# Performance work log

Measured on AMD Instinct MI355X. Metric: run time of the kernel, lower is better.

## Reference

```python
import jax, jax.numpy as jnp
import numpy as np

NUM_LAYERS = 24
LN_EPS = 1e-5


def setup_inputs() -> dict:
    key = jax.random.key(0)
    ks = jax.random.split(key, 8)
    B, S = 256, 8192
    x = jax.random.uniform(ks[0], (B, S, 5), dtype=jnp.float32)
    # per-layer LayerNorm(4) params (torch default init: weight=1, bias=0; use
    # randomized values so the gather is non-trivial)
    ln_w = 1.0 + 0.1 * jax.random.normal(ks[1], (NUM_LAYERS, 4), dtype=jnp.float32)
    ln_b = 0.1 * jax.random.normal(ks[2], (NUM_LAYERS, 4), dtype=jnp.float32)
    # MLP 5 -> 64 -> 32 -> 1 (dropout inactive in eval mode)
    W1 = jax.random.normal(ks[3], (64, 5), dtype=jnp.float32) / np.sqrt(5)
    b1 = jnp.zeros((64,), dtype=jnp.float32)
    W2 = jax.random.normal(ks[4], (32, 64), dtype=jnp.float32) / np.sqrt(64)
    b2 = jnp.zeros((32,), dtype=jnp.float32)
    W3 = jax.random.normal(ks[5], (1, 32), dtype=jnp.float32) / np.sqrt(32)
    b3 = jnp.zeros((1,), dtype=jnp.float32)
    return {"x": x, "ln_w": ln_w, "ln_b": ln_b, "W1": W1, "b1": b1,
            "W2": W2, "b2": b2, "W3": W3, "b3": b3}


def reference(x, ln_w, ln_b, W1, b1, W2, b2, W3, b3):
    B, S, _ = x.shape
    x_flat = x.reshape(-1, 5)                      # [N, 5]
    layer_pos = x_flat[:, -1]                      # [N]
    layer_ids = jnp.clip((layer_pos * NUM_LAYERS).astype(jnp.int32), 0, NUM_LAYERS - 1)
    feats = x_flat[:, :4]                          # [N, 4]
    # vectorized per-token LayerNorm: gather per-token gamma/beta by layer id
    mean = jnp.mean(feats, axis=-1, keepdims=True)
    var = jnp.mean(jnp.square(feats - mean), axis=-1, keepdims=True)  # biased, as torch LN
    normed = (feats - mean) * jax.lax.rsqrt(var + LN_EPS)
    normed = normed * ln_w[layer_ids] + ln_b[layer_ids]               # [N, 4]
    x_norm = jnp.concatenate([normed, layer_pos[:, None]], axis=1)    # [N, 5]
    h = jax.nn.relu(x_norm @ W1.T + b1)            # [N, 64]
    h = jax.nn.relu(h @ W2.T + b2)                 # [N, 32]
    scores = h @ W3.T + b3                         # [N, 1]
    return scores.reshape(B, S)
```

## Files before the change

kernel.cpp:

```cpp
#include <hip/hip_runtime.h>
#include <hip/hip_bf16.h>
#include <stdint.h>

#define NUM_LAYERS 24
#define LN_EPS 1e-5f
#define N_ROWS (256 * 8192)
#define ROWS_PER_ITER 64
#define NUM_ITERS (N_ROWS / ROWS_PER_ITER)
#define NUM_BLOCKS 768

typedef __attribute__((ext_vector_type(4)))  uint32_t u32x4;
typedef __attribute__((ext_vector_type(16))) float    f32x16;
typedef __attribute__((ext_vector_type(2)))  float    f32x2;
typedef __attribute__((ext_vector_type(2)))  __fp16   h16x2;

__device__ __forceinline__ uint32_t pk_f16_rtz(float lo, float hi) {
    h16x2 v = __builtin_amdgcn_cvt_pkrtz(lo, hi);
    uint32_t u; __builtin_memcpy(&u, &v, 4);
    return u;
}
__device__ __forceinline__ uint32_t pk_f16_rne(float lo, float hi) {
    __fp16 a = (__fp16)lo, b = (__fp16)hi;
    uint16_t ua, ub;
    __builtin_memcpy(&ua, &a, 2); __builtin_memcpy(&ub, &b, 2);
    return (uint32_t)ua | ((uint32_t)ub << 16);
}
__device__ __forceinline__ uint32_t pk_relu_f16(uint32_t d) {
    h16x2 v; __builtin_memcpy(&v, &d, 4);
    h16x2 z = {(__fp16)0.0f, (__fp16)0.0f};
    v = __builtin_elementwise_max(v, z);
    uint32_t u; __builtin_memcpy(&u, &v, 4);
    return u;
}

__device__ __forceinline__ u32x4 make_frag(uint32_t d0, uint32_t d1,
                                           uint32_t d2, uint32_t d3) {
    u32x4 f; f.x = d0; f.y = d1; f.z = d2; f.w = d3;
    return f;
}

__device__ __forceinline__ f32x16 mfma_f16_c(u32x4 a, u32x4 b, const f32x16& c) {
    f32x16 d;
    asm("s_nop 2\n\tv_mfma_f32_32x32x16_f16 %0, %1, %2, %3"
        : "=&v"(d) : "v"(a), "v"(b), "v"(c));
    return d;
}
__device__ __forceinline__ f32x16 mfma_f16_z(u32x4 a, u32x4 b) {
    f32x16 d;
    asm("s_nop 2\n\tv_mfma_f32_32x32x16_f16 %0, %1, %2, 0"
        : "=&v"(d) : "v"(a), "v"(b));
    return d;
}
__device__ __forceinline__ void mfma_f16_acc(f32x16& c, u32x4 a, u32x4 b) {
    asm("s_nop 2\n\tv_mfma_f32_32x32x16_f16 %0, %1, %2, %0"
        : "+v"(c) : "v"(a), "v"(b));
}
__device__ __forceinline__ void mfma_fence2(f32x16& c0, f32x16& c1) {
    asm volatile("s_nop 7\n\ts_nop 7\n\ts_nop 7" : "+v"(c0), "+v"(c1));
}
__device__ __forceinline__ void mfma_fence4(f32x16& c0, f32x16& c1,
                                            f32x16& c2, f32x16& c3) {
    asm volatile("s_nop 7\n\ts_nop 7\n\ts_nop 7"
                 : "+v"(c0), "+v"(c1), "+v"(c2), "+v"(c3));
}

__device__ __forceinline__ int sigma_k(int p) {
    int hh = (p >> 2) & 1;
    int base = (p & 31) - 4 * hh;
    int r = (base & 3) + 4 * (base >> 3);
    return 32 * (p >> 5) + 16 * (r >> 3) + 8 * hh + (r & 7);
}

__global__ __launch_bounds__(256, 3) void router_mfma(
    const float* __restrict__ x,
    const float* __restrict__ ln_w,
    const float* __restrict__ ln_b,
    const float* __restrict__ W1,
    const float* __restrict__ b1,
    const float* __restrict__ W2,
    const float* __restrict__ b2,
    const float* __restrict__ W3,
    const float* __restrict__ b3,
    float* __restrict__ out)
{
    __shared__ float s_ln[NUM_LAYERS * 8];
    const int t = threadIdx.x;
    if (t < NUM_LAYERS * 4) {
        int lid = t >> 2, c = t & 3;
        s_ln[lid * 8 + c]     = ln_w[t];
        s_ln[lid * 8 + 4 + c] = ln_b[t];
    }
    __syncthreads();

    const int lane = t & 63;
    const int wid  = t >> 6;
    const int n32  = lane & 31;
    const int h    = lane >> 5;

    u32x4 a1f[2];
#pragma unroll
    for (int mt = 0; mt < 2; ++mt) {
        int p = mt * 32 + n32;
        int k = sigma_k(p);
        uint32_t d0 = pk_f16_rne(W1[k * 5 + 0], W1[k * 5 + 1]);
        uint32_t d1 = pk_f16_rne(W1[k * 5 + 2], W1[k * 5 + 3]);
        uint32_t d2 = pk_f16_rne(W1[k * 5 + 4], b1[k]);
        if (h) { d0 = 0; d1 = 0; d2 = 0; }
        a1f[mt] = make_frag(d0, d1, d2, 0);
    }

    u32x4 w2f[4];
#pragma unroll
    for (int kt = 0; kt < 4; ++kt) {
        const float* wp = W2 + n32 * 64 + kt * 16 + h * 8;
        const float4 lo = *(const float4*)(wp);
        const float4 hi = *(const float4*)(wp + 4);
        w2f[kt] = make_frag(pk_f16_rne(lo.x, lo.y), pk_f16_rne(lo.z, lo.w),
                            pk_f16_rne(hi.x, hi.y), pk_f16_rne(hi.z, hi.w));
    }

    f32x16 c2init;
    f32x2 w3p[8];
#pragma unroll
    for (int r2 = 0; r2 < 8; ++r2) {
        const int n = ((2 * r2) & 3) + 8 * (r2 >> 1) + 4 * h;
        w3p[r2] = f32x2{W3[n], W3[n + 1]};
        c2init[2 * r2]     = b2[n];
        c2init[2 * r2 + 1] = b2[n + 1];
    }
    const float b3v = b3[0];
    const f32x2 z2 = {0.0f, 0.0f};

    const int total_waves = NUM_BLOCKS * 4;
    const int w = blockIdx.x * 4 + wid;

    int it = w;
    const float* xp0 = x + (size_t)(it * ROWS_PER_ITER + lane) * 5;
    float f0 = xp0[0], f1 = xp0[1], f2 = xp0[2], f3 = xp0[3], lp = xp0[4];

    while (true) {
        const int nit = it + total_waves;
        const bool more = nit < NUM_ITERS;
        const float* nxp =
            x + (size_t)((more ? nit : it) * ROWS_PER_ITER + lane) * 5;
        const float nf0 = nxp[0], nf1 = nxp[1], nf2 = nxp[2], nf3 = nxp[3],
                    nlp = nxp[4];

        const int rowBase = it * ROWS_PER_ITER;

        int lid = (int)(lp * (float)NUM_LAYERS);
        lid = lid < 0 ? 0 : (lid > NUM_LAYERS - 1 ? NUM_LAYERS - 1 : lid);

        const float m  = (f0 + f1 + f2 + f3) * 0.25f;
        const float d0 = f0 - m, d1 = f1 - m, d2 = f2 - m, d3 = f3 - m;
        const float var = (d0 * d0 + d1 * d1 + d2 * d2 + d3 * d3) * 0.25f;
        const float r   = rsqrtf(var + LN_EPS);

        const float4 g  = *(const float4*)(s_ln + lid * 8);
        const float4 bb = *(const float4*)(s_ln + lid * 8 + 4);

        const float xn0 = fmaf(d0 * r, g.x, bb.x);
        const float xn1 = fmaf(d1 * r, g.y, bb.y);
        const float xn2 = fmaf(d2 * r, g.z, bb.z);
        const float xn3 = fmaf(d3 * r, g.w, bb.w);

        const uint32_t e0 = pk_f16_rtz(xn0, xn1);
        const uint32_t e1 = pk_f16_rtz(xn2, xn3);
        const uint32_t e2 = pk_f16_rtz(lp, 1.0f);
        const uint32_t x0 = __shfl_xor((int)e0, 32, 64);
        const uint32_t x1 = __shfl_xor((int)e1, 32, 64);
        const uint32_t x2 = __shfl_xor((int)e2, 32, 64);

        const u32x4 bf_t0 = make_frag(e0, e1, e2, 0u);
        const u32x4 bf_t1 = make_frag(x0, x1, x2, 0u);

        f32x16 c1a0 = mfma_f16_z(a1f[0], bf_t0);
        f32x16 c1b0 = mfma_f16_z(a1f[1], bf_t0);
        f32x16 c1a1 = mfma_f16_z(a1f[0], bf_t1);
        f32x16 c1b1 = mfma_f16_z(a1f[1], bf_t1);
        mfma_fence4(c1a0, c1b0, c1a1, c1b1);

        u32x4 h1f0[4], h1f1[4];
#pragma unroll
        for (int kt = 0; kt < 4; ++kt) {
            const f32x16& c1 = (kt < 2) ? c1a0 : c1b0;
            const int roff = 8 * (kt & 1);
            uint32_t dw[4];
#pragma unroll
            for (int d = 0; d < 4; ++d)
                dw[d] = pk_relu_f16(
                    pk_f16_rtz(c1[roff + 2 * d], c1[roff + 2 * d + 1]));
            h1f0[kt] = make_frag(dw[0], dw[1], dw[2], dw[3]);
        }
#pragma unroll
        for (int kt = 0; kt < 4; ++kt) {
            const f32x16& c1 = (kt < 2) ? c1a1 : c1b1;
            const int roff = 8 * (kt & 1);
            uint32_t dw[4];
#pragma unroll
            for (int d = 0; d < 4; ++d)
                dw[d] = pk_relu_f16(
                    pk_f16_rtz(c1[roff + 2 * d], c1[roff + 2 * d + 1]));
            h1f1[kt] = make_frag(dw[0], dw[1], dw[2], dw[3]);
        }

        f32x16 c2_0 = mfma_f16_c(w2f[0], h1f0[0], c2init);
        f32x16 c2_1 = mfma_f16_c(w2f[0], h1f1[0], c2init);
#pragma unroll
        for (int kt = 1; kt < 4; ++kt) {
            mfma_f16_acc(c2_0, w2f[kt], h1f0[kt]);
            mfma_f16_acc(c2_1, w2f[kt], h1f1[kt]);
        }
        mfma_fence2(c2_0, c2_1);

        f32x2 acc0 = z2, acc1 = z2;
#pragma unroll
        for (int r2 = 0; r2 < 8; ++r2) {
            f32x2 v0 = {c2_0[2 * r2], c2_0[2 * r2 + 1]};
            f32x2 v1 = {c2_1[2 * r2], c2_1[2 * r2 + 1]};
            v0 = __builtin_elementwise_max(v0, z2);
            v1 = __builtin_elementwise_max(v1, z2);
            acc0 = v0 * w3p[r2] + acc0;
            acc1 = v1 * w3p[r2] + acc1;
        }
        float p0 = acc0.x + acc0.y;
        float p1 = acc1.x + acc1.y;
        p0 += __shfl_xor(p0, 32, 64);
        p1 += __shfl_xor(p1, 32, 64);

        out[rowBase + lane] = (h ? p1 : p0) + b3v;

        if (!more) break;
        it = nit;
        f0 = nf0; f1 = nf1; f2 = nf2; f3 = nf3; lp = nlp;
    }
}

extern "C" void kernel_launch(void* const* d_in, const int* in_sizes, int n_in,
                              void* d_out, int out_size, void* d_ws, size_t ws_size,
                              hipStream_t stream) {
    const float* x    = (const float*)d_in[0];
    const float* ln_w = (const float*)d_in[1];
    const float* ln_b = (const float*)d_in[2];
    const float* W1   = (const float*)d_in[3];
    const float* b1   = (const float*)d_in[4];
    const float* W2   = (const float*)d_in[5];
    const float* b2   = (const float*)d_in[6];
    const float* W3   = (const float*)d_in[7];
    const float* b3   = (const float*)d_in[8];
    float* out = (float*)d_out;

    router_mfma<<<NUM_BLOCKS, 256, 0, stream>>>(x, ln_w, ln_b, W1, b1, W2, b2,
                                                W3, b3, out);
}
```

Baseline: 108.8 us.

## Coalesce x loads via LDS staging, batch MFMA asm, raise block count

Each wave now loads its 64-row chunk of x with contiguous, coalesced 4-byte loads (stride 64 per pass) and stages it through a per-wave LDS buffer before reading per-row features, instead of strided 5-float per-lane loads. The MFMA calls are merged into two multi-instruction asm blocks so there are fewer s_nop hazard pads, the LayerNorm params are stored transposed in LDS and use the hardware rsq builtin, and the grid grows from 768 to 2048 blocks. This adds LDS traffic, relies on intra-wave ordering of the LDS writes and reads without a barrier, and raises register pressure from the large asm operand lists.

Measured after the change: 108.3 us. No clear change (-0.4%).

```diff
diff --git a/kernel.cpp b/kernel.cpp
--- a/kernel.cpp
+++ b/kernel.cpp
@@ -1,5 +1,4 @@
 #include <hip/hip_runtime.h>
-#include <hip/hip_bf16.h>
 #include <stdint.h>
 
 #define NUM_LAYERS 24
@@ -7,7 +6,7 @@
 #define N_ROWS (256 * 8192)
 #define ROWS_PER_ITER 64
 #define NUM_ITERS (N_ROWS / ROWS_PER_ITER)
-#define NUM_BLOCKS 768
+#define NUM_BLOCKS 2048
 
 typedef __attribute__((ext_vector_type(4)))  uint32_t u32x4;
 typedef __attribute__((ext_vector_type(16))) float    f32x16;
@@ -39,21 +38,38 @@
     return f;
 }
 
-__device__ __forceinline__ f32x16 mfma_f16_c(u32x4 a, u32x4 b, const f32x16& c) {
-    f32x16 d;
-    asm("s_nop 2\n\tv_mfma_f32_32x32x16_f16 %0, %1, %2, %3"
-        : "=&v"(d) : "v"(a), "v"(b), "v"(c));
-    return d;
-}
-__device__ __forceinline__ f32x16 mfma_f16_z(u32x4 a, u32x4 b) {
-    f32x16 d;
-    asm("s_nop 2\n\tv_mfma_f32_32x32x16_f16 %0, %1, %2, 0"
-        : "=&v"(d) : "v"(a), "v"(b));
-    return d;
-}
-__device__ __forceinline__ void mfma_f16_acc(f32x16& c, u32x4 a, u32x4 b) {
-    asm("s_nop 2\n\tv_mfma_f32_32x32x16_f16 %0, %1, %2, %0"
-        : "+v"(c) : "v"(a), "v"(b));
+__device__ __forceinline__ void mfma_l1(f32x16& d0, f32x16& d1,
+                                        f32x16& d2, f32x16& d3,
+                                        const u32x4& a0, const u32x4& a1,
+                                        const u32x4& b0, const u32x4& b1) {
+    asm("s_nop 2\n\t"
+        "v_mfma_f32_32x32x16_f16 %0, %4, %6, 0\n\t"
+        "v_mfma_f32_32x32x16_f16 %1, %5, %6, 0\n\t"
+        "v_mfma_f32_32x32x16_f16 %2, %4, %7, 0\n\t"
+        "v_mfma_f32_32x32x16_f16 %3, %5, %7, 0"
+        : "=&v"(d0), "=&v"(d1), "=&v"(d2), "=&v"(d3)
+        : "v"(a0), "v"(a1), "v"(b0), "v"(b1));
+}
+__device__ __forceinline__ void mfma_l2(f32x16& c0, f32x16& c1, const f32x16& cinit,
+                                        const u32x4& w0, const u32x4& w1,
+                                        const u32x4& w2, const u32x4& w3,
+                                        const u32x4& h00, const u32x4& h01,
+                                        const u32x4& h02, const u32x4& h03,
+                                        const u32x4& h10, const u32x4& h11,
+                                        const u32x4& h12, const u32x4& h13) {
+    asm("s_nop 2\n\t"
+        "v_mfma_f32_32x32x16_f16 %0, %3, %7, %2\n\t"
+        "v_mfma_f32_32x32x16_f16 %1, %3, %11, %2\n\t"
+        "v_mfma_f32_32x32x16_f16 %0, %4, %8, %0\n\t"
+        "v_mfma_f32_32x32x16_f16 %1, %4, %12, %1\n\t"
+        "v_mfma_f32_32x32x16_f16 %0, %5, %9, %0\n\t"
+        "v_mfma_f32_32x32x16_f16 %1, %5, %13, %1\n\t"
+        "v_mfma_f32_32x32x16_f16 %0, %6, %10, %0\n\t"
+        "v_mfma_f32_32x32x16_f16 %1, %6, %14, %1"
+        : "=&v"(c0), "=&v"(c1)
+        : "v"(cinit), "v"(w0), "v"(w1), "v"(w2), "v"(w3),
+          "v"(h00), "v"(h01), "v"(h02), "v"(h03),
+          "v"(h10), "v"(h11), "v"(h12), "v"(h13));
 }
 __device__ __forceinline__ void mfma_fence2(f32x16& c0, f32x16& c1) {
     asm volatile("s_nop 7\n\ts_nop 7\n\ts_nop 7" : "+v"(c0), "+v"(c1));
@@ -83,12 +99,14 @@
     const float* __restrict__ b3,
     float* __restrict__ out)
 {
-    __shared__ float s_ln[NUM_LAYERS * 8];
+    __shared__ float s_ln[8 * NUM_LAYERS];
+    __shared__ float s_x[4][ROWS_PER_ITER * 5];
+
     const int t = threadIdx.x;
-    if (t < NUM_LAYERS * 4) {
-        int lid = t >> 2, c = t & 3;
-        s_ln[lid * 8 + c]     = ln_w[t];
-        s_ln[lid * 8 + 4 + c] = ln_b[t];
+    if (t < 8 * NUM_LAYERS) {
+        const int q = t & 7, lid = t >> 3;
+        s_ln[q * NUM_LAYERS + lid] =
+            (q < 4) ? ln_w[lid * 4 + q] : ln_b[lid * 4 + (q - 4)];
     }
     __syncthreads();
 
@@ -134,17 +152,27 @@
     const int total_waves = NUM_BLOCKS * 4;
     const int w = blockIdx.x * 4 + wid;
 
+    float* const sx = &s_x[wid][0];
+    const float* const sxr = sx + 5 * lane;
+
     int it = w;
-    const float* xp0 = x + (size_t)(it * ROWS_PER_ITER + lane) * 5;
-    float f0 = xp0[0], f1 = xp0[1], f2 = xp0[2], f3 = xp0[3], lp = xp0[4];
+    {
+        const float* xg = x + (size_t)it * (ROWS_PER_ITER * 5);
+        float ld[5];
+#pragma unroll
+        for (int j = 0; j < 5; ++j) ld[j] = xg[j * 64 + lane];
+#pragma unroll
+        for (int j = 0; j < 5; ++j) sx[j * 64 + lane] = ld[j];
+    }
+    float f0 = sxr[0], f1 = sxr[1], f2 = sxr[2], f3 = sxr[3], lp = sxr[4];
 
     while (true) {
         const int nit = it + total_waves;
         const bool more = nit < NUM_ITERS;
-        const float* nxp =
-            x + (size_t)((more ? nit : it) * ROWS_PER_ITER + lane) * 5;
-        const float nf0 = nxp[0], nf1 = nxp[1], nf2 = nxp[2], nf3 = nxp[3],
-                    nlp = nxp[4];
+        const float* xg = x + (size_t)(more ? nit : it) * (ROWS_PER_ITER * 5);
+        float ld[5];
+#pragma unroll
+        for (int j = 0; j < 5; ++j) ld[j] = xg[j * 64 + lane];
 
         const int rowBase = it * ROWS_PER_ITER;
 
@@ -154,15 +182,19 @@
         const float m  = (f0 + f1 + f2 + f3) * 0.25f;
         const float d0 = f0 - m, d1 = f1 - m, d2 = f2 - m, d3 = f3 - m;
         const float var = (d0 * d0 + d1 * d1 + d2 * d2 + d3 * d3) * 0.25f;
-        const float r   = rsqrtf(var + LN_EPS);
-
-        const float4 g  = *(const float4*)(s_ln + lid * 8);
-        const float4 bb = *(const float4*)(s_ln + lid * 8 + 4);
-
-        const float xn0 = fmaf(d0 * r, g.x, bb.x);
-        const float xn1 = fmaf(d1 * r, g.y, bb.y);
-        const float xn2 = fmaf(d2 * r, g.z, bb.z);
-        const float xn3 = fmaf(d3 * r, g.w, bb.w);
+#if __has_builtin(__builtin_amdgcn_rsqf)
+        const float r = __builtin_amdgcn_rsqf(var + LN_EPS);
+#else
+        const float r = rsqrtf(var + LN_EPS);
+#endif
+        const float rg0 = r * s_ln[0 * 24 + lid];
+        const float rg1 = r * s_ln[1 * 24 + lid];
+        const float rg2 = r * s_ln[2 * 24 + lid];
+        const float rg3 = r * s_ln[3 * 24 + lid];
+        const float xn0 = fmaf(d0, rg0, s_ln[4 * 24 + lid]);
+        const float xn1 = fmaf(d1, rg1, s_ln[5 * 24 + lid]);
+        const float xn2 = fmaf(d2, rg2, s_ln[6 * 24 + lid]);
+        const float xn3 = fmaf(d3, rg3, s_ln[7 * 24 + lid]);
 
         const uint32_t e0 = pk_f16_rtz(xn0, xn1);
         const uint32_t e1 = pk_f16_rtz(xn2, xn3);
@@ -174,10 +206,8 @@
         const u32x4 bf_t0 = make_frag(e0, e1, e2, 0u);
         const u32x4 bf_t1 = make_frag(x0, x1, x2, 0u);
 
-        f32x16 c1a0 = mfma_f16_z(a1f[0], bf_t0);
-        f32x16 c1b0 = mfma_f16_z(a1f[1], bf_t0);
-        f32x16 c1a1 = mfma_f16_z(a1f[0], bf_t1);
-        f32x16 c1b1 = mfma_f16_z(a1f[1], bf_t1);
+        f32x16 c1a0, c1b0, c1a1, c1b1;
+        mfma_l1(c1a0, c1b0, c1a1, c1b1, a1f[0], a1f[1], bf_t0, bf_t1);
         mfma_fence4(c1a0, c1b0, c1a1, c1b1);
 
         u32x4 h1f0[4], h1f1[4];
@@ -204,13 +234,11 @@
             h1f1[kt] = make_frag(dw[0], dw[1], dw[2], dw[3]);
         }
 
-        f32x16 c2_0 = mfma_f16_c(w2f[0], h1f0[0], c2init);
-        f32x16 c2_1 = mfma_f16_c(w2f[0], h1f1[0], c2init);
-#pragma unroll
-        for (int kt = 1; kt < 4; ++kt) {
-            mfma_f16_acc(c2_0, w2f[kt], h1f0[kt]);
-            mfma_f16_acc(c2_1, w2f[kt], h1f1[kt]);
-        }
+        f32x16 c2_0, c2_1;
+        mfma_l2(c2_0, c2_1, c2init,
+                w2f[0], w2f[1], w2f[2], w2f[3],
+                h1f0[0], h1f0[1], h1f0[2], h1f0[3],
+                h1f1[0], h1f1[1], h1f1[2], h1f1[3]);
         mfma_fence2(c2_0, c2_1);
 
         f32x2 acc0 = z2, acc1 = z2;
@@ -230,9 +258,12 @@
 
         out[rowBase + lane] = (h ? p1 : p0) + b3v;
 
+#pragma unroll
+        for (int j = 0; j < 5; ++j) sx[j * 64 + lane] = ld[j];
+        f0 = sxr[0]; f1 = sxr[1]; f2 = sxr[2]; f3 = sxr[3]; lp = sxr[4];
+
         if (!more) break;
         it = nit;
-        f0 = nf0; f1 = nf1; f2 = nf2; f3 = nf3; lp = nlp;
     }
 }
 
```
